# Optimization experiments

Hardware: AMD Instinct MI355X
Metric: run time of the kernel (lower is better)

Reference implementation:

```python
import jax, jax.numpy as jnp
import numpy as np

VOCAB = 34004
EMB = 300
UNITS = 512


def setup_inputs() -> dict:
    key = jax.random.key(0)
    ks = jax.random.split(key, 16)
    s = 0.05
    B, T_in, T_out = 64, 60, 31
    inp = {
        "dec_input": jax.random.randint(ks[0], (B, T_out), 0, VOCAB, dtype=jnp.int64 if jax.config.jax_enable_x64 else jnp.int32),
        "h0": jax.random.normal(ks[1], (B, UNITS), jnp.float32),
        "c0": jax.random.normal(ks[2], (B, UNITS), jnp.float32),
        "memory": jax.random.normal(ks[3], (B, T_in, UNITS), jnp.float32),
        # embedding table
        "embedding": jax.random.normal(ks[4], (VOCAB, EMB), jnp.float32) * s,
        # LSTM cell: input = concat(emb, prev_attention) -> EMB + UNITS
        "Wk": jax.random.normal(ks[5], (EMB + UNITS, 4 * UNITS), jnp.float32) * s,
        "Uk": jax.random.normal(ks[6], (UNITS, 4 * UNITS), jnp.float32) * s,
        "bk": jnp.zeros((4 * UNITS,), jnp.float32),
        # Bahdanau attention: memory layer, query layer, score vector v
        "Wm": jax.random.normal(ks[7], (UNITS, UNITS), jnp.float32) * s,
        "Wq": jax.random.normal(ks[8], (UNITS, UNITS), jnp.float32) * s,
        "v_att": jax.random.normal(ks[9], (UNITS,), jnp.float32) * s,
        # attention_layer (Dense(dec_units, use_bias=False)) on concat(cell_out, context)
        "Wa": jax.random.normal(ks[10], (2 * UNITS, UNITS), jnp.float32) * s,
        # output projection fc to vocab
        "Wfc": jax.random.normal(ks[11], (UNITS, VOCAB), jnp.float32) * s,
        "bfc": jnp.zeros((VOCAB,), jnp.float32),
    }
    return inp


def reference(dec_input, h0, c0, memory, embedding, Wk, Uk, bk, Wm, Wq, v_att, Wa, Wfc, bfc):
    # Teacher-forced (training=True) AttentionWrapper decode with Bahdanau attention.
    keys = jnp.einsum("btd,de->bte", memory, Wm)  # precompute memory projection [B,T_in,U]
    emb = embedding[dec_input]                      # [B,T_out,EMB]
    emb_t = jnp.swapaxes(emb, 0, 1)                 # [T_out,B,EMB]
    attn0 = jnp.zeros_like(h0)                      # initial attention is zeros

    def step(carry, e):
        h, c, attn = carry
        x = jnp.concatenate([e, attn], axis=-1)     # default cell_input_fn: concat
        z = x @ Wk + h @ Uk + bk                    # [B,4U]
        i, f, g, o = jnp.split(z, 4, axis=-1)       # keras LSTM gate order i,f,c,o
        i = jax.nn.sigmoid(i); f = jax.nn.sigmoid(f)
        g = jnp.tanh(g); o = jax.nn.sigmoid(o)
        c_new = f * c + i * g
        h_new = o * jnp.tanh(c_new)
        # Bahdanau score: v^T tanh(W_m*memory + W_q*query)
        q = h_new @ Wq                               # [B,U]
        score = jnp.einsum("btu,u->bt", jnp.tanh(keys + q[:, None, :]), v_att)
        align = jax.nn.softmax(score, axis=-1)       # [B,T_in]
        context = jnp.einsum("bt,btd->bd", align, memory)
        attn_new = jnp.concatenate([h_new, context], axis=-1) @ Wa  # attention_layer
        logits = attn_new @ Wfc + bfc                # output_layer (fc)
        return (h_new, c_new, attn_new), logits

    _, logits = jax.lax.scan(step, (h0, c0, attn0), emb_t)
    return jnp.swapaxes(logits, 0, 1)               # [B, T_out, vocab] = rnn_output
```

## Files before the change

### kernel.cpp

```cpp
#include <hip/hip_runtime.h>
#include <cstdint>
#include <cstddef>

typedef _Float16 f16;
typedef _Float16 f16x8 __attribute__((ext_vector_type(8)));
typedef float    f32x4 __attribute__((ext_vector_type(4)));
typedef uint32_t u32x4 __attribute__((ext_vector_type(4)));

#define DEV static __device__ __forceinline__

constexpr int TOUT = 31;
constexpr int VOC  = 34004;
constexpr int VOCP = 34048;

constexpr size_t OFF_SYNC  = 0;
constexpr size_t OFF_MEM16 = 8192;
constexpr size_t OFF_WMSWZ = OFF_MEM16 + (size_t)3840*512*2;
constexpr size_t OFF_KEYS  = OFF_WMSWZ + (size_t)16*512*32*2;
constexpr size_t OFF_EMBA  = OFF_KEYS  + (size_t)3840*512*2;
constexpr size_t OFF_WKTOP = OFF_EMBA  + (size_t)1984*320*2;
constexpr size_t OFF_EMBW  = OFF_WKTOP + (size_t)10*2048*32*2;
constexpr size_t OFF_WA16  = OFF_EMBW  + (size_t)1984*2048*4;
constexpr size_t OFF_WKATT = OFF_WA16  + (size_t)1024*512*2;
constexpr size_t OFF_WCA   = OFF_WKATT + (size_t)16*2048*32*2;
constexpr size_t OFF_WSTAR = OFF_WCA   + (size_t)1024*2048*4;
constexpr size_t OFF_UK16  = OFF_WSTAR + (size_t)32*2048*32*2;
constexpr size_t OFF_WQSWZ = OFF_UK16  + (size_t)16*2048*32*2;
constexpr size_t OFF_WASWZ = OFF_WQSWZ + (size_t)512*512*2;
constexpr size_t OFF_H016  = OFF_WASWZ + (size_t)32*512*32*2;
constexpr size_t OFF_YALL  = OFF_H016  + (size_t)64*512*2;
constexpr size_t OFF_ATT16 = OFF_YALL  + (size_t)31*64*1024*2;
constexpr size_t OFF_BKP   = OFF_ATT16 + (size_t)1984*512*2;
constexpr size_t OFF_WFC   = OFF_BKP   + 8192;
constexpr size_t OFF_QP    = OFF_EMBA;

DEV void gload16(const void* src, void* ldsbase ) {
  __builtin_amdgcn_global_load_lds(
      (const __attribute__((address_space(1))) unsigned int*)src,
      (__attribute__((address_space(3))) unsigned int*)ldsbase, 16, 0, 0);
}

DEV float sigm(float x)      { return 1.f / (1.f + expf(-x)); }
DEV float tanh_fast(float x) { float e = __expf(2.f*x); return 1.f - 2.f/(e+1.f); }

DEV uint32_t aload_u32(const uint32_t* p){ return __hip_atomic_load(p, __ATOMIC_RELAXED, __HIP_MEMORY_SCOPE_AGENT); }
DEV void astore_u32(uint32_t* p, uint32_t v){ __hip_atomic_store(p, v, __ATOMIC_RELAXED, __HIP_MEMORY_SCOPE_AGENT); }

DEV void ld16_sc1(const void* p, u32x4& d){
  asm volatile("global_load_dwordx4 %0, %1, off sc1" : "=v"(d) : "v"(p));
}
DEV void st16_sc1(void* p, u32x4 v){
  asm volatile("global_store_dwordx4 %0, %1, off sc1" :: "v"(p), "v"(v) : "memory");
}
DEV void vwait(){ asm volatile("s_waitcnt vmcnt(0)" ::: "memory"); }

__global__ void prep_all(char* ws, const int* dec, const float* h0, const float* memory,
                         const float* embt, const float* Wa, const float* bk,
                         const float* Wm, const float* Wk, const float* Uk, const float* Wq)
{
  const int blk = blockIdx.x, tid = threadIdx.x;

  if (blk < 464) {
    int tg = blk*256 + tid;
    constexpr int S0=8192, S1=S0+20480, S2=S1+32768, S3=S2+32768, S4=S3+16384, S5=S4+8192;
    if (tg >= S5) return;
    f16 buf[32];
    f16* dst;
    if (tg < S0) {
      int kt=tg>>9, n=tg&511;
      #pragma unroll
      for (int kk=0;kk<32;kk++) buf[kk] = (f16)Wm[(size_t)(kt*32+kk)*512 + n];
      dst = (f16*)(ws+OFF_WMSWZ) + (size_t)tg*32;
    } else if (tg < S1) {
      int j=tg-S0; int kt=j>>11, np=j&2047; int col=(np>>2)+(np&3)*512;
      #pragma unroll
      for (int kk=0;kk<32;kk++){ int k=kt*32+kk;
        buf[kk] = (k<300) ? (f16)Wk[(size_t)k*2048+col] : (f16)0.f; }
      dst = (f16*)(ws+OFF_WKTOP) + (size_t)j*32;
    } else if (tg < S2) {
      int j=tg-S1; int kt=j>>11, np=j&2047; int col=(np>>2)+(np&3)*512;
      #pragma unroll
      for (int kk=0;kk<32;kk++) buf[kk] = (f16)Wk[(size_t)(300+kt*32+kk)*2048+col];
      dst = (f16*)(ws+OFF_WKATT) + (size_t)j*32;
    } else if (tg < S3) {
      int j=tg-S2; int kt=j>>11, np=j&2047; int col=(np>>2)+(np&3)*512;
      #pragma unroll
      for (int kk=0;kk<32;kk++) buf[kk] = (f16)Uk[(size_t)(kt*32+kk)*2048+col];
      dst = (f16*)(ws+OFF_UK16) + (size_t)j*32;
    } else if (tg < S4) {
      int j=tg-S3; int kt=j>>9, n=j&511;
      #pragma unroll
      for (int kk=0;kk<32;kk++) buf[kk] = (f16)Wa[(size_t)(kt*32+kk)*512 + n];
      dst = (f16*)(ws+OFF_WASWZ) + (size_t)j*32;
    } else {
      int j=tg-S4; int rr=j>>9, n=j&511;
      #pragma unroll
      for (int kk=0;kk<32;kk++) buf[kk] = (f16)Wq[(size_t)(rr*32+kk)*512 + n];
      dst = (f16*)(ws+OFF_WQSWZ) + (size_t)j*32;
    }
    f16x8* d8 = (f16x8*)dst; f16x8* s8 = (f16x8*)buf;
    d8[0]=s8[0]; d8[1]=s8[1]; d8[2]=s8[2]; d8[3]=s8[3];
    return;
  }

  f16* mem16 = (f16*)(ws+OFF_MEM16);
  f16* embA  = (f16*)(ws+OFF_EMBA);
  f16* wa16  = (f16*)(ws+OFF_WA16);
  f16* h016  = (f16*)(ws+OFF_H016);
  float* bkp = (float*)(ws+OFF_BKP);
  constexpr int E0=1966080, E1=E0+634880, E2=E1+524288, E3=E2+32768, E4=E3+2048;
  for (int i = (blk-464)*256 + tid; i < E4; i += 512*256) {
    if (i < E0) { mem16[i] = (f16)memory[i]; }
    else if (i < E1) { int j=i-E0; int r=j/320, k=j-r*320; int t=r>>6, b=r&63;
      int tok = dec[b*TOUT+t];
      embA[j] = (k<300) ? (f16)embt[(size_t)tok*300+k] : (f16)0.f; }
    else if (i < E2) { int j=i-E1; wa16[j] = (f16)Wa[j]; }
    else if (i < E3) { int j=i-E2; h016[j] = (f16)h0[j]; }
    else { int j=i-E3; bkp[j] = bk[(j>>2) + (j&3)*512]; }
  }
}

__global__ __launch_bounds__(256, 1)
void gemm3(char* ws)
{
  constexpr int BM=128, BN=64, NT=256, AM=4, AN=2, NLA=2, NLB=1;
  __shared__ __align__(16) f16 sA[BM*32];
  __shared__ __align__(16) f16 sB[BN*32];

  const int blk = blockIdx.x, tid = threadIdx.x;
  const int wave = tid>>6, lane = tid&63;
  const int lg = lane>>4, lr = lane&15;

  const f16* A; int lda; const f16* Bs; int Np; void* C; const float* bias = nullptr;
  int bx, by, K, Mreal, mode;
  if (blk < 240) {
    bx = blk & 7; by = blk >> 3;
    A=(const f16*)(ws+OFF_MEM16); lda=512; Bs=(const f16*)(ws+OFF_WMSWZ); Np=512;
    C=ws+OFF_KEYS; K=512; Mreal=3840; mode=1;
  } else if (blk < 752) {
    int i=blk-240; bx=i&31; by=i>>5;
    A=(const f16*)(ws+OFF_EMBA); lda=320; Bs=(const f16*)(ws+OFF_WKTOP); Np=2048;
    C=ws+OFF_EMBW; bias=(const float*)(ws+OFF_BKP); K=320; Mreal=1984; mode=0;
  } else {
    int i=blk-752; bx=i&31; by=i>>5;
    A=(const f16*)(ws+OFF_WA16); lda=512; Bs=(const f16*)(ws+OFF_WKATT); Np=2048;
    C=ws+OFF_WCA; K=512; Mreal=1024; mode=0;
  }
  const int m0 = by*BM, n0 = bx*BN;
  const int wm = (wave>>1)*64, wn = (wave&1)*32;

  f32x4 acc[AM][AN] = {};
  int aoff[AM], boff[AN];
  #pragma unroll
  for (int i=0;i<AM;i++){ int row = wm+i*16+lr; aoff[i] = row*64 + (((lg + (row>>1))&3)<<4); }
  #pragma unroll
  for (int i=0;i<AN;i++){ int row = wn+i*16+lr; boff[i] = row*64 + (((lg + (row>>1))&3)<<4); }

  const int ksteps = K/32;
  for (int ks=0; ks<ksteps; ks++){
    const int k0 = ks*32;
    __syncthreads();
    #pragma unroll
    for (int i=0;i<NLA;i++){
      int p = i*NT + tid;
      int row = p>>2; int g = ((p&3) - (row>>1)) & 3;
      int gm = m0+row; if (gm > Mreal-1) gm = Mreal-1;
      gload16(A + (size_t)gm*lda + k0 + g*8, (char*)sA + (i*NT + wave*64)*16);
    }
    #pragma unroll
    for (int i=0;i<NLB;i++){
      int p = i*NT + tid;
      int row = p>>2; int g = ((p&3) - (row>>1)) & 3;
      gload16(Bs + ((size_t)(k0>>5)*Np + (n0+row))*32 + g*8, (char*)sB + (i*NT + wave*64)*16);
    }
    __syncthreads();
    f16x8 af[AM], bf[AN];
    #pragma unroll
    for (int i=0;i<AM;i++) af[i] = *(const f16x8*)((const char*)sA + aoff[i]);
    #pragma unroll
    for (int i=0;i<AN;i++) bf[i] = *(const f16x8*)((const char*)sB + boff[i]);
    #pragma unroll
    for (int i=0;i<AM;i++)
      #pragma unroll
      for (int j=0;j<AN;j++)
        acc[i][j] = __builtin_amdgcn_mfma_f32_16x16x32_f16(af[i], bf[j], acc[i][j], 0,0,0);
  }

  #pragma unroll
  for (int i=0;i<AM;i++)
    #pragma unroll
    for (int j=0;j<AN;j++){
      int n = n0 + wn + j*16 + lr;
      float bb = (mode == 0 && bias) ? bias[n] : 0.f;
      #pragma unroll
      for (int r=0;r<4;r++){
        int m = m0 + wm + i*16 + lg*4 + r;
        if (m >= Mreal) continue;
        float v = acc[i][j][r] + bb;
        if (mode == 0) ((float*)C)[(size_t)m*Np + n] = v;
        else           ((f16*)C)[(size_t)m*Np + n] = (f16)v;
      }
    }
}

__global__ void build_wstar(char* ws, const float* Uk)
{
  int tg = blockIdx.x*256 + threadIdx.x;
  int kt = tg>>11, np = tg&2047;
  int col = (np>>2)+(np&3)*512;
  const float* wca = (const float*)(ws+OFF_WCA);
  f16 buf[32];
  #pragma unroll
  for (int kk=0;kk<32;kk++){
    int k = kt*32+kk;
    float v = wca[(size_t)k*2048 + np];
    if (k < 512) v += Uk[(size_t)k*2048 + col];
    buf[kk] = (f16)v;
  }
  f16* dst = (f16*)(ws+OFF_WSTAR) + (size_t)tg*32;
  f16x8* d8 = (f16x8*)dst; f16x8* s8 = (f16x8*)buf;
  d8[0]=s8[0]; d8[1]=s8[1]; d8[2]=s8[2]; d8[3]=s8[3];
}

template<int BM, int BN, int WR, int WC, int MODE>
__global__ __launch_bounds__(WR*WC*64, 1)
void gemm16(const f16* __restrict__ A, int lda,
            const f16* __restrict__ Bs, int Np,
            void* __restrict__ C, const float* __restrict__ bias,
            int M, int K, int Mreal, int Nreal)
{
  constexpr int NT  = WR*WC*64;
  constexpr int WTM = BM/WR, WTN = BN/WC, AM = WTM/16, AN = WTN/16;
  constexpr int NLA = BM*64/(NT*16), NLB = BN*64/(NT*16);
  __shared__ __align__(16) f16 sA[BM*32];
  __shared__ __align__(16) f16 sB[BN*32];
  const int tid = threadIdx.x, wave = tid>>6, lane = tid&63;
  const int lg = lane>>4, lr = lane&15;
  const int m0 = blockIdx.y*BM, n0 = blockIdx.x*BN;
  const int wm = (wave/WC)*WTM, wn = (wave%WC)*WTN;

  f32x4 acc[AM][AN] = {};

  int aoff[AM], boff[AN];
  #pragma unroll
  for (int i=0;i<AM;i++){ int row = wm+i*16+lr; aoff[i] = row*64 + (((lg + (row>>1))&3)<<4); }
  #pragma unroll
  for (int i=0;i<AN;i++){ int row = wn+i*16+lr; boff[i] = row*64 + (((lg + (row>>1))&3)<<4); }

  const int ksteps = K/32;
  for (int ks=0; ks<ksteps; ks++){
    const int k0 = ks*32;
    __syncthreads();
    #pragma unroll
    for (int i=0;i<NLA;i++){
      int p = i*NT + tid;
      int row = p>>2; int g = ((p&3) - (row>>1)) & 3;
      int gm = m0+row; if (gm > Mreal-1) gm = Mreal-1;
      gload16(A + (size_t)gm*lda + k0 + g*8, (char*)sA + (i*NT + wave*64)*16);
    }
    #pragma unroll
    for (int i=0;i<NLB;i++){
      int p = i*NT + tid;
      int row = p>>2; int g = ((p&3) - (row>>1)) & 3;
      gload16(Bs + ((size_t)(k0>>5)*Np + (n0+row))*32 + g*8, (char*)sB + (i*NT + wave*64)*16);
    }
    __syncthreads();
    f16x8 af[AM], bf[AN];
    #pragma unroll
    for (int i=0;i<AM;i++) af[i] = *(const f16x8*)((const char*)sA + aoff[i]);
    #pragma unroll
    for (int i=0;i<AN;i++) bf[i] = *(const f16x8*)((const char*)sB + boff[i]);
    #pragma unroll
    for (int i=0;i<AM;i++)
      #pragma unroll
      for (int j=0;j<AN;j++)
        acc[i][j] = __builtin_amdgcn_mfma_f32_16x16x32_f16(af[i], bf[j], acc[i][j], 0,0,0);
  }

  #pragma unroll
  for (int i=0;i<AM;i++)
    #pragma unroll
    for (int j=0;j<AN;j++){
      int n = n0 + wn + j*16 + lr;
      if (MODE == 2 && n >= Nreal) continue;
      float bb = 0.f;
      if (MODE != 1 && bias) bb = bias[n];
      #pragma unroll
      for (int r=0;r<4;r++){
        int m = m0 + wm + i*16 + lg*4 + r;
        if (m >= Mreal) continue;
        float v = acc[i][j][r] + bb;
        if (MODE == 0)      ((float*)C)[(size_t)m*Np + n] = v;
        else if (MODE == 1) ((f16*)C)[(size_t)m*Np + n] = (f16)v;
        else { int t = m>>6, b = m&63; ((float*)C)[((size_t)(b*TOUT+t))*VOC + n] = v; }
      }
    }
}

__global__ __launch_bounds__(512, 1)
void gemm_logits(const f16* __restrict__ A,
                 const f16* __restrict__ Bs,
                 float* __restrict__ out, const float* __restrict__ bias)
{
  constexpr int BM=256, BN=128, NT=512, AM=4, AN=4, NLA=2, NLB=1;
  __shared__ __align__(16) f16 sA[BM*32];
  __shared__ __align__(16) f16 sB[BN*32];
  const int tid = threadIdx.x, wave = tid>>6, lane = tid&63;
  const int lg = lane>>4, lr = lane&15;

  const int flat = (blockIdx.x & 7)*266 + (blockIdx.x >> 3);
  const int bx = flat >> 3, by = flat & 7;
  const int m0 = by*BM, n0 = bx*BN;
  const int wm = (wave/2)*64, wn = (wave&1)*64;

  f32x4 acc[AM][AN] = {};

  int aoff[AM], boff[AN];
  #pragma unroll
  for (int i=0;i<AM;i++){ int row = wm+i*16+lr; aoff[i] = row*64 + (((lg + (row>>1))&3)<<4); }
  #pragma unroll
  for (int i=0;i<AN;i++){ int row = wn+i*16+lr; boff[i] = row*64 + (((lg + (row>>1))&3)<<4); }

  for (int ks=0; ks<16; ks++){
    const int k0 = ks*32;
    __syncthreads();
    #pragma unroll
    for (int i=0;i<NLA;i++){
      int p = i*NT + tid;
      int row = p>>2; int g = ((p&3) - (row>>1)) & 3;
      int gm = m0+row; if (gm > 1983) gm = 1983;
      gload16(A + (size_t)gm*512 + k0 + g*8, (char*)sA + (i*NT + wave*64)*16);
    }
    {
      int p = tid;
      int row = p>>2; int g = ((p&3) - (row>>1)) & 3;
      gload16(Bs + ((size_t)ks*VOCP + (n0+row))*32 + g*8, (char*)sB + (wave*64)*16);
    }
    __syncthreads();
    f16x8 af[AM], bf[AN];
    #pragma unroll
    for (int i=0;i<AM;i++) af[i] = *(const f16x8*)((const char*)sA + aoff[i]);
    #pragma unroll
    for (int i=0;i<AN;i++) bf[i] = *(const f16x8*)((const char*)sB + boff[i]);
    #pragma unroll
    for (int i=0;i<AM;i++)
      #pragma unroll
      for (int j=0;j<AN;j++)
        acc[i][j] = __builtin_amdgcn_mfma_f32_16x16x32_f16(af[i], bf[j], acc[i][j], 0,0,0);
  }

  #pragma unroll
  for (int i=0;i<AM;i++)
    #pragma unroll
    for (int j=0;j<AN;j++){
      int n = n0 + wn + j*16 + lr;
      if (n >= VOC) continue;
      float bb = bias[n];
      #pragma unroll
      for (int r=0;r<4;r++){
        int m = m0 + wm + i*16 + lg*4 + r;
        if (m >= 1984) continue;
        int t = m>>6, b = m&63;
        out[((size_t)(b*TOUT+t))*VOC + n] = acc[i][j][r] + bb;
      }
    }
}

DEV void cbar(uint32_t* flags, int cbase, int r, int tid, uint32_t target)
{
  vwait();
  __syncthreads();
  if (tid == 0)
    astore_u32(flags + (size_t)(cbase + r)*32, target);
  if (tid < 16) {
    while (aload_u32(flags + (size_t)(cbase + tid)*32) < target)
      __builtin_amdgcn_s_sleep(1);
  }
  __syncthreads();
}

template<int KS>
DEV f32x4 p1_mfma(const f16* __restrict__ Bs, const char* ylb, int col, int kg, int lr)
{
  f16x8 B[8];
  #pragma unroll
  for (int i=0;i<8;i++)
    B[i] = *(const f16x8*)(Bs + (((size_t)i*2048 + col)<<5) + kg*8);
  f32x4 acc = {};
  #pragma unroll
  for (int ks=0; ks<KS; ks+=8) {
    #pragma unroll
    for (int i=0;i<8;i++) {
      f16x8 a = *(const f16x8*)(ylb + lr*2064 + (ks+i)*64 + kg*16);
      acc = __builtin_amdgcn_mfma_f32_16x16x32_f16(a, B[i], acc, 0,0,0);
      int nk = ks+8+i;
      if (nk < KS)
        B[i] = *(const f16x8*)(Bs + (((size_t)nk*2048 + col)<<5) + kg*8);
    }
  }
  return acc;
}

__global__ __launch_bounds__(512, 1)
void recur_wfc(char* ws, const float* __restrict__ c0, const float* __restrict__ v_att,
               const float* __restrict__ Wfc)
{
  const int blk = blockIdx.x, tid = threadIdx.x;

  if (blk >= 64) {
    const int cb = blk - 64;
    const int n = cb*256 + (tid & 255);
    const int kt0 = (tid >> 8) * 8;
    if (n < VOCP) {
      f16* wdst = (f16*)(ws+OFF_WFC);
      for (int kt = kt0; kt < kt0+8; kt++) {
        f16 buf[32];
        #pragma unroll
        for (int kk=0;kk<32;kk++)
          buf[kk] = (n < VOC) ? (f16)Wfc[(size_t)(kt*32+kk)*VOC + n] : (f16)0.f;
        f16x8* d8 = (f16x8*)((f16*)wdst + ((size_t)kt*VOCP + n)*32);
        f16x8* s8 = (f16x8*)buf;
        d8[0]=s8[0]; d8[1]=s8[1]; d8[2]=s8[2]; d8[3]=s8[3];
      }
    }
    return;
  }

  const int wave = tid>>6, lane = tid&63;
  const int lr = lane&15, kg = lane>>4;
  const int clus = blk>>4, r = blk&15;
  const int cbase = clus<<4;
  const int bown = cbase + r;
  const int n0 = r*128;

  uint32_t* flags = (uint32_t*)(ws+OFF_SYNC);
  char* qpg = (char*)(ws+OFF_QP);
  const f16* wstar = (const f16*)(ws+OFF_WSTAR);
  const f16* uk16  = (const f16*)(ws+OFF_UK16);
  const f16* wqswz = (const f16*)(ws+OFF_WQSWZ);
  const f16* keys16= (const f16*)(ws+OFF_KEYS);
  const f16* mem16 = (const f16*)(ws+OFF_MEM16);
  const float* embw= (const float*)(ws+OFF_EMBW);

  __shared__ __align__(16) char  ybuf[33024];
  __shared__ __align__(16) float zl[16*132];
  __shared__ __align__(16) float c_sl[512];
  __shared__ __align__(16) f16   h_sl[512];
  __shared__ __align__(16) float q_l[512];
  __shared__ __align__(16) float v_l[512];
  __shared__ __align__(16) f16   cx16_l[512];
  __shared__ __align__(16) float sc_l[64];
  __shared__ __align__(16) f16   mem_lds[60*512];

  v_l[tid] = v_att[tid];
  { int b = tid>>5, uu = tid&31;
    c_sl[tid] = c0[(size_t)(cbase+b)*512 + r*32 + uu]; }

  {
    const char* msrc = (const char*)(mem16 + (size_t)bown*60*512);
    #pragma unroll
    for (int i=0;i<8;i++){
      int cb2 = i*512 + wave*64;
      if (cb2 < 3840)
        gload16(msrc + ((size_t)cb2 + lane)*16, (char*)mem_lds + (size_t)cb2*16);
    }
  }

  for (int t=0; t<TOUT; t++){
    {
      const char* ysrc; int rsh;
      if (t == 0) { ysrc = ws+OFF_H016; rsh = 6; }
      else        { ysrc = ws+OFF_YALL + (size_t)(t-1)*64*2048; rsh = 7; }
      const int npass = (16 << rsh) >> 9;
      u32x4 g[4];
      #pragma unroll
      for (int p=0;p<4;p++){
        if (p < npass){
          int cid = p*512 + tid, row = cid>>rsh, off = cid & ((1<<rsh)-1);
          ld16_sc1(ysrc + ((size_t)(cbase+row) << (rsh+4)) + off*16, g[p]);
        }
      }
      vwait();
      #pragma unroll
      for (int p=0;p<4;p++){
        if (p < npass){
          int cid = p*512 + tid, row = cid>>rsh, off = cid & ((1<<rsh)-1);
          *(u32x4*)(ybuf + row*2064 + off*16) = g[p];
        }
      }
      __syncthreads();
    }

    {
      const int col = n0 + wave*16 + lr;
      f32x4 acc = (t==0) ? p1_mfma<16>(uk16,  ybuf, col, kg, lr)
                         : p1_mfma<32>(wstar, ybuf, col, kg, lr);
      #pragma unroll
      for (int rr=0;rr<4;rr++)
        zl[(kg*4+rr)*132 + wave*16 + lr] = acc[rr];
    }
    __syncthreads();

    {
      const int b = tid>>5, uu = tid&31;
      f32x4 zz = *(const f32x4*)(zl + b*132 + uu*4);
      f32x4 e  = *(const f32x4*)(embw + ((size_t)(t*64+cbase+b))*2048 + n0 + uu*4);
      float ig = sigm(zz[0]+e[0]), fg = sigm(zz[1]+e[1]);
      float gg = tanhf(zz[2]+e[2]), og = sigm(zz[3]+e[3]);
      float cn = fg*c_sl[tid] + ig*gg;
      c_sl[tid] = cn;
      h_sl[tid] = (f16)(og * tanhf(cn));
    }
    __syncthreads();

    char* yt = (char*)(ws+OFF_YALL) + (size_t)t*64*2048;
    if (tid < 64){
      int b = tid>>2, off = tid&3;
      u32x4 v = *(const u32x4*)((const char*)h_sl + b*64 + off*16);
      st16_sc1(yt + (size_t)(cbase+b)*2048 + r*64 + off*16, v);
    }

    {
      float* qs = (float*)ybuf;
      f16x8 a = *(const f16x8*)(h_sl + lr*32 + kg*8);
      #pragma unroll
      for (int j=0;j<4;j++){
        int n = wave*64 + j*16 + lr;
        f16x8 bf = *(const f16x8*)(wqswz + ((size_t)(r*512 + n))*32 + kg*8);
        f32x4 aq = __builtin_amdgcn_mfma_f32_16x16x32_f16(a, bf, (f32x4){0.f,0.f,0.f,0.f}, 0,0,0);
        #pragma unroll
        for (int rr=0;rr<4;rr++)
          qs[(kg*4+rr)*512 + n] = aq[rr];
      }
    }
    __syncthreads();
    {
      #pragma unroll
      for (int p=0;p<4;p++){
        int cid = p*512 + tid;
        u32x4 v = *(const u32x4*)(ybuf + cid*16);
        st16_sc1(qpg + (size_t)blk*32768 + cid*16, v);
      }
    }
    cbar(flags, cbase, r, tid, 2*t+1);

    {
      u32x4 gq[4];
      #pragma unroll
      for (int p=0;p<4;p++){
        int cid = p*512 + tid, s = cid>>7, off = cid&127;
        ld16_sc1(qpg + (size_t)(cbase+s)*32768 + r*2048 + off*16, gq[p]);
      }
      vwait();
      #pragma unroll
      for (int p=0;p<4;p++){
        int cid = p*512 + tid;
        *(u32x4*)(ybuf + cid*16) = gq[p];
      }
      __syncthreads();
      const float* qin = (const float*)ybuf;
      float qsum = 0.f;
      #pragma unroll
      for (int s=0;s<16;s++) qsum += qin[s*512 + tid];
      q_l[tid] = qsum;
    }
    __syncthreads();

    for (int i = wave; i < 60; i += 8){
      const f16* krow = keys16 + ((size_t)(bown*60+i))*512;
      float p = 0.f;
      #pragma unroll
      for (int s=0;s<8;s++){
        int u = lane + s*64;
        p += tanh_fast((float)krow[u] + q_l[u]) * v_l[u];
      }
      #pragma unroll
      for (int m=32;m;m>>=1) p += __shfl_xor(p, m, 64);
      if (lane == 0) sc_l[i] = p;
    }
    __syncthreads();
    if (wave == 0){
      float s = (lane < 60) ? sc_l[lane] : -1e30f;
      float mx = s;
      #pragma unroll
      for (int m=32;m;m>>=1) mx = fmaxf(mx, __shfl_xor(mx, m, 64));
      float ev = (lane < 60) ? __expf(s - mx) : 0.f;
      float sum = ev;
      #pragma unroll
      for (int m=32;m;m>>=1) sum += __shfl_xor(sum, m, 64);
      if (lane < 60) sc_l[lane] = ev / sum;
    }
    __syncthreads();
    {
      float cx = 0.f;
      #pragma unroll
      for (int i=0;i<60;i++) cx += sc_l[i] * (float)mem_lds[i*512 + tid];
      cx16_l[tid] = (f16)cx;
    }
    __syncthreads();
    if (tid < 64){
      u32x4 v = *(const u32x4*)((const char*)cx16_l + tid*16);
      st16_sc1(yt + (size_t)bown*2048 + 1024 + tid*16, v);
    }
    cbar(flags, cbase, r, tid, 2*t+2);
  }
}

extern "C" void kernel_launch(void* const* d_in, const int* in_sizes, int n_in,
                              void* d_out, int out_size, void* d_ws, size_t ws_size,
                              hipStream_t stream)
{
  const int*   dec  = (const int*)  d_in[0];
  const float* h0   = (const float*)d_in[1];
  const float* c0   = (const float*)d_in[2];
  const float* mem  = (const float*)d_in[3];
  const float* embt = (const float*)d_in[4];
  const float* Wk   = (const float*)d_in[5];
  const float* Uk   = (const float*)d_in[6];
  const float* bk   = (const float*)d_in[7];
  const float* Wm   = (const float*)d_in[8];
  const float* Wq   = (const float*)d_in[9];
  const float* va   = (const float*)d_in[10];
  const float* Wa   = (const float*)d_in[11];
  const float* Wfc  = (const float*)d_in[12];
  const float* bfc  = (const float*)d_in[13];
  char* ws = (char*)d_ws;

  hipMemsetAsync(ws + OFF_SYNC, 0, 8192, stream);

  prep_all<<<976, 256, 0, stream>>>(ws, dec, h0, mem, embt, Wa, bk, Wm, Wk, Uk, Wq);
  gemm3<<<1008, 256, 0, stream>>>(ws);
  build_wstar<<<256, 256, 0, stream>>>(ws, Uk);

  recur_wfc<<<204, 512, 0, stream>>>(ws, c0, va, Wfc);

  gemm16<128,64,2,2,1><<<dim3(8,16), 256, 0, stream>>>(
      (const f16*)(ws+OFF_YALL), 1024, (const f16*)(ws+OFF_WASWZ), 512,
      ws+OFF_ATT16, nullptr, 1984, 1024, 1984, 512);

  gemm_logits<<<2128, 512, 0, stream>>>(
      (const f16*)(ws+OFF_ATT16), (const f16*)(ws+OFF_WFC), (float*)d_out, bfc);
}
```

Baseline: 764.6 us.

## Move Wfc conversion into gemm3 and process two K-slices per logits sync

The Wfc fp32-to-fp16 swizzled conversion moves out of the recurrence launch, where it ran as extra side blocks, into extra blocks of the earlier gemm3 launch. The recurrence kernel now launches only its 64 persistent blocks. The logits GEMM also stages two 32-wide K slices per barrier pair, halving the number of __syncthreads and doubling shared memory. The intent is to cut contention during the latency-bound recurrence and reduce barrier overhead in the logits GEMM, at the risk of lengthening gemm3 and raising LDS use.

```diff
diff --git a/kernel.cpp b/kernel.cpp
--- a/kernel.cpp
+++ b/kernel.cpp
@@ -121,13 +121,32 @@
 }
 
 __global__ __launch_bounds__(256, 1)
-void gemm3(char* ws)
+void gemm3(char* ws, const float* __restrict__ Wfc)
 {
   constexpr int BM=128, BN=64, NT=256, AM=4, AN=2, NLA=2, NLB=1;
   __shared__ __align__(16) f16 sA[BM*32];
   __shared__ __align__(16) f16 sB[BN*32];
 
   const int blk = blockIdx.x, tid = threadIdx.x;
+
+  if (blk >= 1008) {
+    const int cb = blk - 1008;
+    const int n = cb*256 + tid;
+    if (n < VOCP) {
+      f16* wdst = (f16*)(ws+OFF_WFC);
+      for (int kt = 0; kt < 16; kt++) {
+        f16 buf[32];
+        #pragma unroll
+        for (int kk=0;kk<32;kk++)
+          buf[kk] = (n < VOC) ? (f16)Wfc[(size_t)(kt*32+kk)*VOC + n] : (f16)0.f;
+        f16x8* d8 = (f16x8*)(wdst + ((size_t)kt*VOCP + n)*32);
+        f16x8* s8 = (f16x8*)buf;
+        d8[0]=s8[0]; d8[1]=s8[1]; d8[2]=s8[2]; d8[3]=s8[3];
+      }
+    }
+    return;
+  }
+
   const int wave = tid>>6, lane = tid&63;
   const int lg = lane>>4, lr = lane&15;
 
@@ -302,9 +321,9 @@
                  const f16* __restrict__ Bs,
                  float* __restrict__ out, const float* __restrict__ bias)
 {
-  constexpr int BM=256, BN=128, NT=512, AM=4, AN=4, NLA=2, NLB=1;
-  __shared__ __align__(16) f16 sA[BM*32];
-  __shared__ __align__(16) f16 sB[BN*32];
+  constexpr int BM=256, BN=128, NT=512, AM=4, AN=4;
+  __shared__ __align__(16) f16 sA[2][BM*32];
+  __shared__ __align__(16) f16 sB[2][BN*32];
   const int tid = threadIdx.x, wave = tid>>6, lane = tid&63;
   const int lg = lane>>4, lr = lane&15;
 
@@ -321,32 +340,38 @@
   #pragma unroll
   for (int i=0;i<AN;i++){ int row = wn+i*16+lr; boff[i] = row*64 + (((lg + (row>>1))&3)<<4); }
 
-  for (int ks=0; ks<16; ks++){
-    const int k0 = ks*32;
-    __syncthreads();
-    #pragma unroll
-    for (int i=0;i<NLA;i++){
-      int p = i*NT + tid;
-      int row = p>>2; int g = ((p&3) - (row>>1)) & 3;
-      int gm = m0+row; if (gm > 1983) gm = 1983;
-      gload16(A + (size_t)gm*512 + k0 + g*8, (char*)sA + (i*NT + wave*64)*16);
-    }
-    {
-      int p = tid;
-      int row = p>>2; int g = ((p&3) - (row>>1)) & 3;
-      gload16(Bs + ((size_t)ks*VOCP + (n0+row))*32 + g*8, (char*)sB + (wave*64)*16);
-    }
-    __syncthreads();
-    f16x8 af[AM], bf[AN];
-    #pragma unroll
-    for (int i=0;i<AM;i++) af[i] = *(const f16x8*)((const char*)sA + aoff[i]);
-    #pragma unroll
-    for (int i=0;i<AN;i++) bf[i] = *(const f16x8*)((const char*)sB + boff[i]);
-    #pragma unroll
-    for (int i=0;i<AM;i++)
-      #pragma unroll
-      for (int j=0;j<AN;j++)
-        acc[i][j] = __builtin_amdgcn_mfma_f32_16x16x32_f16(af[i], bf[j], acc[i][j], 0,0,0);
+  for (int ks2=0; ks2<8; ks2++){
+    __syncthreads();
+    #pragma unroll
+    for (int h=0; h<2; h++){
+      const int k0 = ks2*64 + h*32;
+      #pragma unroll
+      for (int i=0;i<2;i++){
+        int p = i*NT + tid;
+        int row = p>>2; int g = ((p&3) - (row>>1)) & 3;
+        int gm = m0+row; if (gm > 1983) gm = 1983;
+        gload16(A + (size_t)gm*512 + k0 + g*8, (char*)sA[h] + (i*NT + wave*64)*16);
+      }
+      {
+        int p = tid;
+        int row = p>>2; int g = ((p&3) - (row>>1)) & 3;
+        gload16(Bs + ((size_t)(ks2*2+h)*VOCP + (n0+row))*32 + g*8, (char*)sB[h] + (wave*64)*16);
+      }
+    }
+    __syncthreads();
+    #pragma unroll
+    for (int h=0; h<2; h++){
+      f16x8 af[AM], bf[AN];
+      #pragma unroll
+      for (int i=0;i<AM;i++) af[i] = *(const f16x8*)((const char*)sA[h] + aoff[i]);
+      #pragma unroll
+      for (int j=0;j<AN;j++) bf[j] = *(const f16x8*)((const char*)sB[h] + boff[j]);
+      #pragma unroll
+      for (int i=0;i<AM;i++)
+        #pragma unroll
+        for (int j=0;j<AN;j++)
+          acc[i][j] = __builtin_amdgcn_mfma_f32_16x16x32_f16(af[i], bf[j], acc[i][j], 0,0,0);
+    }
   }
 
   #pragma unroll
@@ -402,30 +427,9 @@
 }
 
 __global__ __launch_bounds__(512, 1)
-void recur_wfc(char* ws, const float* __restrict__ c0, const float* __restrict__ v_att,
-               const float* __restrict__ Wfc)
+void recur(char* ws, const float* __restrict__ c0, const float* __restrict__ v_att)
 {
   const int blk = blockIdx.x, tid = threadIdx.x;
-
-  if (blk >= 64) {
-    const int cb = blk - 64;
-    const int n = cb*256 + (tid & 255);
-    const int kt0 = (tid >> 8) * 8;
-    if (n < VOCP) {
-      f16* wdst = (f16*)(ws+OFF_WFC);
-      for (int kt = kt0; kt < kt0+8; kt++) {
-        f16 buf[32];
-        #pragma unroll
-        for (int kk=0;kk<32;kk++)
-          buf[kk] = (n < VOC) ? (f16)Wfc[(size_t)(kt*32+kk)*VOC + n] : (f16)0.f;
-        f16x8* d8 = (f16x8*)((f16*)wdst + ((size_t)kt*VOCP + n)*32);
-        f16x8* s8 = (f16x8*)buf;
-        d8[0]=s8[0]; d8[1]=s8[1]; d8[2]=s8[2]; d8[3]=s8[3];
-      }
-    }
-    return;
-  }
-
   const int wave = tid>>6, lane = tid&63;
   const int lr = lane&15, kg = lane>>4;
   const int clus = blk>>4, r = blk&15;
@@ -629,10 +633,12 @@
   hipMemsetAsync(ws + OFF_SYNC, 0, 8192, stream);
 
   prep_all<<<976, 256, 0, stream>>>(ws, dec, h0, mem, embt, Wa, bk, Wm, Wk, Uk, Wq);
-  gemm3<<<1008, 256, 0, stream>>>(ws);
+
+  gemm3<<<1141, 256, 0, stream>>>(ws, Wfc);
+
   build_wstar<<<256, 256, 0, stream>>>(ws, Uk);
 
-  recur_wfc<<<204, 512, 0, stream>>>(ws, c0, va, Wfc);
+  recur<<<64, 512, 0, stream>>>(ws, c0, va);
 
   gemm16<128,64,2,2,1><<<dim3(8,16), 256, 0, stream>>>(
       (const f16*)(ws+OFF_YALL), 1024, (const f16*)(ws+OFF_WASWZ), 512,
```

Result: slower. 974.5 us (+27.5%).
